# Kernel optimization log

Measured on AMD Instinct MI355X. Metric: run time of the kernel, lower is better.

## Reference

```python
import jax, jax.numpy as jnp
import numpy as np

EPS = 1e-3  # keras LayerNormalization default epsilon

def layernorm(x, gamma, beta):
    mu = jnp.mean(x, axis=-1, keepdims=True)
    var = jnp.var(x, axis=-1, keepdims=True)
    return (x - mu) * jax.lax.rsqrt(var + EPS) * gamma + beta

def setup_inputs() -> dict:
    key = jax.random.key(0)
    ks = jax.random.split(key, 20)
    B, N, T, Dimg, H = 512, 100, 14, 2048, 768
    s = lambda k, *sh: jax.random.normal(k, sh, dtype=jnp.float32) * 0.02
    return {
        "img_feat": jax.random.normal(ks[0], (B, N, Dimg), dtype=jnp.float32),
        "ques_feat": jax.random.normal(ks[1], (B, T, H), dtype=jnp.float32),
        "Wc": s(ks[2], Dimg, H), "bc": jnp.zeros((H,), jnp.float32),
        "Wq": s(ks[3], H, H),    "bq": jnp.zeros((H,), jnp.float32),
        "Wi": s(ks[4], Dimg, H), "bi": jnp.zeros((H,), jnp.float32),
        "wqa": s(ks[5], H, 1), "bqa": jnp.zeros((1,), jnp.float32),
        "wia": s(ks[6], H, 1), "bia": jnp.zeros((1,), jnp.float32),
        "g1": jnp.ones((N,), jnp.float32), "b1": jnp.zeros((N,), jnp.float32),
        "g2": jnp.ones((H,), jnp.float32), "b2": jnp.zeros((H,), jnp.float32),
        "g3": jnp.ones((T,), jnp.float32), "b3": jnp.zeros((T,), jnp.float32),
        "g4": jnp.ones((H,), jnp.float32), "b4": jnp.zeros((H,), jnp.float32),
        "g5": jnp.ones((N,), jnp.float32), "b5": jnp.zeros((N,), jnp.float32),
    }

def reference(img_feat, ques_feat, Wc, bc, Wq, bq, Wi, bi, wqa, bqa, wia, bia,
              g1, b1, g2, b2, g3, b3, g4, b4, g5, b5):
    # img_feat: [B,N,Dimg], ques_feat: [B,T,H]
    img_corr = img_feat @ Wc + bc                                   # [B,N,H]
    wm = jnp.einsum('bth,bnh->btn', ques_feat, img_corr)            # [B,T,N]
    wm = jax.nn.relu(layernorm(wm, g1, b1))
    ques_embed = ques_feat @ Wq + bq                                # [B,T,H]
    img_embed = img_feat @ Wi + bi                                  # [B,N,H]
    transform_img = jnp.einsum('btn,bnh->bth', wm, img_embed)       # [B,T,H]
    ques_atten_sum = jax.nn.relu(layernorm(transform_img + ques_embed, g2, b2))
    # dropout is identity at inference
    ques_atten = (ques_atten_sum @ wqa + bqa)[..., 0]               # [B,T]
    ques_atten = jax.nn.softmax(layernorm(ques_atten, g3, b3), axis=-1)
    transform_ques = jnp.einsum('btn,bth->bnh', wm, ques_embed)     # [B,N,H]
    img_atten_sum = jax.nn.relu(layernorm(transform_ques + img_embed, g4, b4))
    img_atten = (img_atten_sum @ wia + bia)[..., 0]                 # [B,N]
    img_atten = jax.nn.softmax(layernorm(img_atten, g5, b5), axis=-1)
    ques_atten_feat = jnp.einsum('bt,bth->bh', ques_atten, ques_feat)  # [B,H]
    img_atten_feat = jnp.einsum('bn,bnd->bd', img_atten, img_feat)     # [B,Dimg]
    return (img_atten_feat, ques_atten_feat)
```

## Files before the change

kernel.cpp:

```cpp
#include <hip/hip_runtime.h>

using f32x4     = __attribute__((ext_vector_type(4))) float;
using bf16x8    = __attribute__((ext_vector_type(8))) short;
using ushort4_t = __attribute__((ext_vector_type(4))) unsigned short;
using ushort8_t = __attribute__((ext_vector_type(8))) unsigned short;
using uint4_t   = __attribute__((ext_vector_type(4))) unsigned int;

__device__ __forceinline__ unsigned short f2bf(float f) {
    unsigned u = __builtin_bit_cast(unsigned, f);
    u += 0x7fffu + ((u >> 16) & 1u);
    return (unsigned short)(u >> 16);
}

__device__ __forceinline__ float wave_sum(float v) {
#pragma unroll
    for (int off = 32; off > 0; off >>= 1) v += __shfl_xor(v, off, 64);
    return v;
}
__device__ __forceinline__ float wave_max(float v) {
#pragma unroll
    for (int off = 32; off > 0; off >>= 1) v = fmaxf(v, __shfl_xor(v, off, 64));
    return v;
}

#define GLP(p)  ((const __attribute__((address_space(1))) void*)(p))
#define LDSP(p) ((__attribute__((address_space(3))) void*)(p))

__global__ __launch_bounds__(256) void cvt_bf16(const float* __restrict__ in,
                                                unsigned short* __restrict__ out, long n8) {
    long i = (long)blockIdx.x * 256 + threadIdx.x;
    long stride = (long)gridDim.x * 256;
    for (; i < n8; i += stride) {
        const float4* p = (const float4*)(in + i * 8);
        float4 a = p[0], b = p[1];
        ushort8_t v;
        v[0] = f2bf(a.x); v[1] = f2bf(a.y); v[2] = f2bf(a.z); v[3] = f2bf(a.w);
        v[4] = f2bf(b.x); v[5] = f2bf(b.y); v[6] = f2bf(b.z); v[7] = f2bf(b.w);
        *(ushort8_t*)(out + i * 8) = v;
    }
}

__global__ void pack_w(const float* __restrict__ Wc, const float* __restrict__ Wi,
                       unsigned short* __restrict__ Wp) {
    int n = blockIdx.x, k = blockIdx.y * 256 + threadIdx.x;
    float v = (n < 768) ? Wc[(size_t)k * 768 + n] : Wi[(size_t)k * 768 + (n - 768)];
    Wp[(size_t)n * 2048 + k] = f2bf(v);
}

__global__ void pack_wq(const float* __restrict__ Wq, unsigned short* __restrict__ Wqt) {
    int n = blockIdx.x, k = blockIdx.y * 256 + threadIdx.x;
    Wqt[(size_t)n * 768 + k] = f2bf(Wq[(size_t)k * 768 + n]);
}

__global__ __launch_bounds__(512, 1) void gemm8(
    const unsigned short* __restrict__ A, const unsigned short* __restrict__ Bt,
    const float* __restrict__ bias0, const float* __restrict__ bias1, int nsplit,
    float* __restrict__ C, int N, int K, int NTN)
{
    __shared__ unsigned short LA[4][8192];
    __shared__ unsigned short LB[4][8192];
    const int tid = threadIdx.x, lane = tid & 63, wid = tid >> 6;

    int nwg = (int)gridDim.x, bid = (int)blockIdx.x;
    if ((nwg & 7) == 0) { int cpx = nwg >> 3; bid = (bid & 7) * cpx + (bid >> 3); }
    const int tn = bid % NTN, tm = bid / NTN;
    const size_t m0 = (size_t)tm * 256, n0 = (size_t)tn * 256;
    const int NT = K >> 5;

    const int wr = wid >> 2, wc = wid & 3;
    const int wm = wr * 128, wn = wc * 64;
    const int fr = lane & 15, fs = lane >> 4;

    const int c0 = tid, c1 = tid + 512;
    const int r0 = c0 >> 2, s0 = ((c0 & 3) - (r0 >> 1)) & 3;
    const int r1 = c1 >> 2, s1 = ((c1 & 3) - (r1 >> 1)) & 3;
    const unsigned short* gA0 = A + (m0 + r0) * K + s0 * 8;
    const unsigned short* gA1 = A + (m0 + r1) * K + s1 * 8;
    const unsigned short* gB0 = Bt + (n0 + r0) * K + s0 * 8;
    const unsigned short* gB1 = Bt + (n0 + r1) * K + s1 * 8;

    int offA[8], offB[4];
#pragma unroll
    for (int mf = 0; mf < 8; ++mf) {
        int r = wm + mf * 16 + fr;
        offA[mf] = (4 * r + ((fs + (r >> 1)) & 3)) * 8;
    }
#pragma unroll
    for (int nf = 0; nf < 4; ++nf) {
        int r = wn + nf * 16 + fr;
        offB[nf] = (4 * r + ((fs + (r >> 1)) & 3)) * 8;
    }

    f32x4 acc[8][4];
#pragma unroll
    for (int i = 0; i < 8; ++i)
#pragma unroll
        for (int j = 0; j < 4; ++j) acc[i][j] = (f32x4){0.f, 0.f, 0.f, 0.f};

#pragma unroll
    for (int t = 0; t < 3; ++t) {
        if (t < NT) {
            __builtin_amdgcn_global_load_lds(GLP(gA0 + t * 32), LDSP(&LA[t][c0 * 8]), 16, 0, 0);
            __builtin_amdgcn_global_load_lds(GLP(gA1 + t * 32), LDSP(&LA[t][c1 * 8]), 16, 0, 0);
            __builtin_amdgcn_global_load_lds(GLP(gB0 + t * 32), LDSP(&LB[t][c0 * 8]), 16, 0, 0);
            __builtin_amdgcn_global_load_lds(GLP(gB1 + t * 32), LDSP(&LB[t][c1 * 8]), 16, 0, 0);
        }
    }

    for (int T = 0; T < NT; ++T) {
        const int buf = T & 3, pb = (T + 3) & 3;
        const int rem = NT - 1 - T;
        if (rem >= 2)      asm volatile("s_waitcnt vmcnt(8)" ::: "memory");
        else if (rem == 1) asm volatile("s_waitcnt vmcnt(4)" ::: "memory");
        else               asm volatile("s_waitcnt vmcnt(0)" ::: "memory");
        __builtin_amdgcn_s_barrier();
        __builtin_amdgcn_sched_barrier(0);

        bf16x8 av[4], bv[4];
#pragma unroll
        for (int mf = 0; mf < 4; ++mf) av[mf] = *(const bf16x8*)&LA[buf][offA[mf]];
#pragma unroll
        for (int nf = 0; nf < 4; ++nf) bv[nf] = *(const bf16x8*)&LB[buf][offB[nf]];
        if (T + 3 < NT) {
            __builtin_amdgcn_global_load_lds(GLP(gA0 + (size_t)(T + 3) * 32), LDSP(&LA[pb][c0 * 8]), 16, 0, 0);
            __builtin_amdgcn_global_load_lds(GLP(gA1 + (size_t)(T + 3) * 32), LDSP(&LA[pb][c1 * 8]), 16, 0, 0);
        }
        asm volatile("s_waitcnt lgkmcnt(0)" ::: "memory");
        __builtin_amdgcn_sched_barrier(0);
        __builtin_amdgcn_s_setprio(1);
#pragma unroll
        for (int mf = 0; mf < 4; ++mf)
#pragma unroll
            for (int nf = 0; nf < 4; ++nf)
                acc[mf][nf] = __builtin_amdgcn_mfma_f32_16x16x32_bf16(av[mf], bv[nf], acc[mf][nf], 0, 0, 0);
        __builtin_amdgcn_s_setprio(0);

#pragma unroll
        for (int mf = 0; mf < 4; ++mf) av[mf] = *(const bf16x8*)&LA[buf][offA[4 + mf]];
        if (T + 3 < NT) {
            __builtin_amdgcn_global_load_lds(GLP(gB0 + (size_t)(T + 3) * 32), LDSP(&LB[pb][c0 * 8]), 16, 0, 0);
            __builtin_amdgcn_global_load_lds(GLP(gB1 + (size_t)(T + 3) * 32), LDSP(&LB[pb][c1 * 8]), 16, 0, 0);
        }
        asm volatile("s_waitcnt lgkmcnt(0)" ::: "memory");
        __builtin_amdgcn_sched_barrier(0);
        __builtin_amdgcn_s_setprio(1);
#pragma unroll
        for (int mf = 0; mf < 4; ++mf)
#pragma unroll
            for (int nf = 0; nf < 4; ++nf)
                acc[4 + mf][nf] = __builtin_amdgcn_mfma_f32_16x16x32_bf16(av[mf], bv[nf], acc[4 + mf][nf], 0, 0, 0);
        __builtin_amdgcn_s_setprio(0);
    }

#pragma unroll
    for (int nf = 0; nf < 4; ++nf) {
        int col = (int)n0 + wn + nf * 16 + fr;
        float bs = (col < nsplit) ? bias0[col] : bias1[col - nsplit];
#pragma unroll
        for (int mf = 0; mf < 8; ++mf) {
            size_t rowb = m0 + wm + mf * 16 + fs * 4;
#pragma unroll
            for (int r = 0; r < 4; ++r)
                C[(rowb + r) * N + col] = acc[mf][nf][r] + bs;
        }
    }
}

__global__ __launch_bounds__(256) void gemm_fb(
    const float* __restrict__ A, const unsigned short* __restrict__ Bt,
    const float* __restrict__ bias0, const float* __restrict__ bias1, int nsplit,
    float* __restrict__ C, int M, int N, int K)
{
    const int tid = threadIdx.x, lane = tid & 63, wid = tid >> 6;
    const int m0 = blockIdx.x * 128, n0 = blockIdx.y * 128;
    __shared__ unsigned short Al[128 * 40];
    __shared__ unsigned short Bl[128 * 40];

    f32x4 acc[4][4];
#pragma unroll
    for (int i = 0; i < 4; ++i)
#pragma unroll
        for (int j = 0; j < 4; ++j) acc[i][j] = (f32x4){0.f, 0.f, 0.f, 0.f};

    const int wm_ = (wid >> 1) * 64, wn_ = (wid & 1) * 64;
    const int fr = lane & 15, fk = (lane >> 4) * 8;

    for (int k0 = 0; k0 < K; k0 += 32) {
        __syncthreads();
#pragma unroll
        for (int it = 0; it < 4; ++it) {
            int idx = tid + it * 256;
            int row = idx >> 3, c4 = idx & 7;
            float4 v = *(const float4*)(A + (size_t)(m0 + row) * K + k0 + c4 * 4);
            ushort4_t h;
            h.x = f2bf(v.x); h.y = f2bf(v.y); h.z = f2bf(v.z); h.w = f2bf(v.w);
            *(ushort4_t*)&Al[row * 40 + c4 * 4] = h;
        }
#pragma unroll
        for (int it = 0; it < 2; ++it) {
            int idx = tid + it * 256;
            int row = idx >> 2, c4 = idx & 3;
            uint4_t v = *(const uint4_t*)(Bt + (size_t)(n0 + row) * K + k0 + c4 * 8);
            *(uint4_t*)&Bl[row * 40 + c4 * 8] = v;
        }
        __syncthreads();

        bf16x8 af[4], bfr[4];
#pragma unroll
        for (int i = 0; i < 4; ++i) af[i]  = *(const bf16x8*)&Al[(wm_ + i * 16 + fr) * 40 + fk];
#pragma unroll
        for (int j = 0; j < 4; ++j) bfr[j] = *(const bf16x8*)&Bl[(wn_ + j * 16 + fr) * 40 + fk];
#pragma unroll
        for (int i = 0; i < 4; ++i)
#pragma unroll
            for (int j = 0; j < 4; ++j)
                acc[i][j] = __builtin_amdgcn_mfma_f32_16x16x32_bf16(af[i], bfr[j], acc[i][j], 0, 0, 0);
    }

#pragma unroll
    for (int j = 0; j < 4; ++j) {
        int col = n0 + wn_ + j * 16 + (lane & 15);
        float bs = (col < nsplit) ? bias0[col] : bias1[col - nsplit];
#pragma unroll
        for (int i = 0; i < 4; ++i) {
            int rowb = m0 + wm_ + i * 16 + (lane >> 4) * 4;
#pragma unroll
            for (int r = 0; r < 4; ++r)
                C[(size_t)(rowb + r) * N + col] = acc[i][j][r] + bs;
        }
    }
}

__global__ __launch_bounds__(256) void wm_kernel(
    const float* __restrict__ qf_g, const float* __restrict__ imgCE,
    const float* __restrict__ g1, const float* __restrict__ b1,
    float* __restrict__ wm_g)
{
    const int b = blockIdx.x, tid = threadIdx.x, lane = tid & 63, wid = tid >> 6;
    __shared__ float qf[14 * 768];
    __shared__ float wmr[14][100];

    const float4* src = (const float4*)(qf_g + (size_t)b * 14 * 768);
    for (int i = tid; i < 14 * 768 / 4; i += 256) ((float4*)qf)[i] = src[i];
    __syncthreads();

    for (int n = wid; n < 100; n += 4) {
        const float* row = imgCE + ((size_t)b * 100 + n) * 1536;
        float r[12];
#pragma unroll
        for (int j = 0; j < 12; ++j) r[j] = row[lane + 64 * j];
        for (int t = 0; t < 14; ++t) {
            const float* q = qf + t * 768;
            float s = 0.f;
#pragma unroll
            for (int j = 0; j < 12; ++j) s = fmaf(r[j], q[lane + 64 * j], s);
            s = wave_sum(s);
            if (lane == 0) wmr[t][n] = s;
        }
    }
    __syncthreads();

    for (int t = wid; t < 14; t += 4) {
        float x0 = wmr[t][lane];
        float x1 = (lane + 64 < 100) ? wmr[t][lane + 64] : 0.f;
        float s = wave_sum(x0 + x1);
        float q = wave_sum(x0 * x0 + x1 * x1);
        float mu = s * (1.f / 100.f);
        float var = q * (1.f / 100.f) - mu * mu;
        float rs = rsqrtf(var + 1e-3f);
        float* dst = wm_g + ((size_t)b * 14 + t) * 100;
        {
            float v = (x0 - mu) * rs * g1[lane] + b1[lane];
            dst[lane] = v > 0.f ? v : 0.f;
        }
        if (lane + 64 < 100) {
            float v = (x1 - mu) * rs * g1[lane + 64] + b1[lane + 64];
            dst[lane + 64] = v > 0.f ? v : 0.f;
        }
    }
}

__global__ __launch_bounds__(256) void ques_kernel(
    const float* __restrict__ qf_g, const float* __restrict__ qe_g,
    const float* __restrict__ imgCE, const float* __restrict__ wm_g,
    const float* __restrict__ g2, const float* __restrict__ b2,
    const float* __restrict__ g3, const float* __restrict__ b3,
    const float* __restrict__ wqa, const float* __restrict__ bqa,
    float* __restrict__ out_q)
{
    const int b = blockIdx.x, tid = threadIdx.x, lane = tid & 63, wid = tid >> 6;
    __shared__ float qe[14 * 768];
    __shared__ float wm[14 * 100];
    __shared__ float red[4][28];
    __shared__ float mu_s[14], rs_s[14], qa_s[14], qw_s[14];

    {
        const float4* src = (const float4*)(qe_g + (size_t)b * 14 * 768);
        for (int i = tid; i < 14 * 768 / 4; i += 256) ((float4*)qe)[i] = src[i];
        const float* ws = wm_g + (size_t)b * 1400;
        for (int i = tid; i < 1400; i += 256) wm[i] = ws[i];
    }
    __syncthreads();

    float a0[14], a1[14], a2[14];
#pragma unroll
    for (int t = 0; t < 14; ++t) { a0[t] = 0.f; a1[t] = 0.f; a2[t] = 0.f; }

    const float* ie_base = imgCE + (size_t)b * 100 * 1536 + 768;
    for (int n = 0; n < 100; ++n) {
        const float* ie = ie_base + (size_t)n * 1536;
        float e0 = ie[tid], e1 = ie[tid + 256], e2 = ie[tid + 512];
#pragma unroll
        for (int t = 0; t < 14; ++t) {
            float w = wm[t * 100 + n];
            a0[t] = fmaf(w, e0, a0[t]); a1[t] = fmaf(w, e1, a1[t]); a2[t] = fmaf(w, e2, a2[t]);
        }
    }
#pragma unroll
    for (int t = 0; t < 14; ++t) {
        a0[t] += qe[t * 768 + tid];
        a1[t] += qe[t * 768 + tid + 256];
        a2[t] += qe[t * 768 + tid + 512];
    }
#pragma unroll
    for (int t = 0; t < 14; ++t) {
        float s = wave_sum(a0[t] + a1[t] + a2[t]);
        float q = wave_sum(a0[t] * a0[t] + a1[t] * a1[t] + a2[t] * a2[t]);
        if (lane == 0) { red[wid][t] = s; red[wid][14 + t] = q; }
    }
    __syncthreads();
    if (tid < 14) {
        float s = red[0][tid] + red[1][tid] + red[2][tid] + red[3][tid];
        float q = red[0][14 + tid] + red[1][14 + tid] + red[2][14 + tid] + red[3][14 + tid];
        float mu = s * (1.f / 768.f);
        float var = q * (1.f / 768.f) - mu * mu;
        mu_s[tid] = mu; rs_s[tid] = rsqrtf(var + 1e-3f);
    }
    __syncthreads();

    float ga = g2[tid], ba = b2[tid], gb = g2[tid + 256], bb = b2[tid + 256],
          gc = g2[tid + 512], bc_ = b2[tid + 512];
    float w0 = wqa[tid], w1 = wqa[tid + 256], w2 = wqa[tid + 512];
#pragma unroll
    for (int t = 0; t < 14; ++t) {
        float mu = mu_s[t], rs = rs_s[t];
        float v0 = fmaxf((a0[t] - mu) * rs * ga + ba, 0.f);
        float v1 = fmaxf((a1[t] - mu) * rs * gb + bb, 0.f);
        float v2 = fmaxf((a2[t] - mu) * rs * gc + bc_, 0.f);
        float p = wave_sum(v0 * w0 + v1 * w1 + v2 * w2);
        if (lane == 0) red[wid][t] = p;
    }
    __syncthreads();
    if (tid < 14) qa_s[tid] = red[0][tid] + red[1][tid] + red[2][tid] + red[3][tid] + bqa[0];
    __syncthreads();
    if (tid == 0) {
        float s = 0.f;
        for (int t = 0; t < 14; ++t) s += qa_s[t];
        float mu = s * (1.f / 14.f);
        float q = 0.f;
        for (int t = 0; t < 14; ++t) { float d = qa_s[t] - mu; q += d * d; }
        float rs = rsqrtf(q * (1.f / 14.f) + 1e-3f);
        float e[14], mx = -1e30f;
        for (int t = 0; t < 14; ++t) { e[t] = (qa_s[t] - mu) * rs * g3[t] + b3[t]; mx = fmaxf(mx, e[t]); }
        float se = 0.f;
        for (int t = 0; t < 14; ++t) { e[t] = expf(e[t] - mx); se += e[t]; }
        float inv = 1.f / se;
        for (int t = 0; t < 14; ++t) qw_s[t] = e[t] * inv;
    }
    __syncthreads();

    const float* qf = qf_g + (size_t)b * 14 * 768;
#pragma unroll
    for (int c = 0; c < 3; ++c) {
        int h = tid + c * 256;
        float o = 0.f;
#pragma unroll
        for (int t = 0; t < 14; ++t) o = fmaf(qw_s[t], qf[t * 768 + h], o);
        out_q[(size_t)b * 768 + h] = o;
    }
}

__global__ __launch_bounds__(256) void img_kernel(
    const float* __restrict__ img_feat, const float* __restrict__ qe_g,
    const float* __restrict__ imgCE, const float* __restrict__ wm_g,
    const float* __restrict__ g4, const float* __restrict__ b4,
    const float* __restrict__ g5, const float* __restrict__ b5,
    const float* __restrict__ wia, const float* __restrict__ bia,
    float* __restrict__ out_i)
{
    const int b = blockIdx.x, tid = threadIdx.x, lane = tid & 63, wid = tid >> 6;
    __shared__ float qe[14 * 768];
    __shared__ float wm[14 * 100];
    __shared__ float red[4][20];
    __shared__ float mu_s[10], rs_s[10];
    __shared__ float ia_s[100], iw_s[100];

    {
        const float4* src = (const float4*)(qe_g + (size_t)b * 14 * 768);
        for (int i = tid; i < 14 * 768 / 4; i += 256) ((float4*)qe)[i] = src[i];
        const float* ws = wm_g + (size_t)b * 1400;
        for (int i = tid; i < 1400; i += 256) wm[i] = ws[i];
    }
    __syncthreads();

    float g4a = g4[tid], b4a = b4[tid], g4b = g4[tid + 256], b4b = b4[tid + 256],
          g4c = g4[tid + 512], b4c = b4[tid + 512];
    float wa = wia[tid], wb = wia[tid + 256], wc_ = wia[tid + 512];

    for (int g = 0; g < 10; ++g) {
        float t0[10], t1[10], t2[10];
#pragma unroll
        for (int i = 0; i < 10; ++i) { t0[i] = 0.f; t1[i] = 0.f; t2[i] = 0.f; }
#pragma unroll
        for (int t = 0; t < 14; ++t) {
            float q0 = qe[t * 768 + tid], q1 = qe[t * 768 + tid + 256], q2 = qe[t * 768 + tid + 512];
#pragma unroll
            for (int i = 0; i < 10; ++i) {
                float w = wm[t * 100 + g * 10 + i];
                t0[i] = fmaf(w, q0, t0[i]); t1[i] = fmaf(w, q1, t1[i]); t2[i] = fmaf(w, q2, t2[i]);
            }
        }
#pragma unroll
        for (int i = 0; i < 10; ++i) {
            const float* ie = imgCE + ((size_t)b * 100 + g * 10 + i) * 1536 + 768;
            t0[i] += ie[tid]; t1[i] += ie[tid + 256]; t2[i] += ie[tid + 512];
            float s = wave_sum(t0[i] + t1[i] + t2[i]);
            float q = wave_sum(t0[i] * t0[i] + t1[i] * t1[i] + t2[i] * t2[i]);
            if (lane == 0) { red[wid][i] = s; red[wid][10 + i] = q; }
        }
        __syncthreads();
        if (tid < 10) {
            float s = red[0][tid] + red[1][tid] + red[2][tid] + red[3][tid];
            float q = red[0][10 + tid] + red[1][10 + tid] + red[2][10 + tid] + red[3][10 + tid];
            float mu = s * (1.f / 768.f);
            float var = q * (1.f / 768.f) - mu * mu;
            mu_s[tid] = mu; rs_s[tid] = rsqrtf(var + 1e-3f);
        }
        __syncthreads();
#pragma unroll
        for (int i = 0; i < 10; ++i) {
            float mu = mu_s[i], rs = rs_s[i];
            float v0 = fmaxf((t0[i] - mu) * rs * g4a + b4a, 0.f);
            float v1 = fmaxf((t1[i] - mu) * rs * g4b + b4b, 0.f);
            float v2 = fmaxf((t2[i] - mu) * rs * g4c + b4c, 0.f);
            float p = wave_sum(v0 * wa + v1 * wb + v2 * wc_);
            if (lane == 0) red[wid][i] = p;
        }
        __syncthreads();
        if (tid < 10) ia_s[g * 10 + tid] = red[0][tid] + red[1][tid] + red[2][tid] + red[3][tid] + bia[0];
        __syncthreads();
    }

    if (wid == 0) {
        float x0 = ia_s[lane];
        float x1 = (lane + 64 < 100) ? ia_s[lane + 64] : 0.f;
        float s = wave_sum(x0 + x1);
        float q = wave_sum(x0 * x0 + x1 * x1);
        float mu = s * 0.01f;
        float var = q * 0.01f - mu * mu;
        float rs = rsqrtf(var + 1e-3f);
        float v0 = (x0 - mu) * rs * g5[lane] + b5[lane];
        float v1 = (lane + 64 < 100) ? (x1 - mu) * rs * g5[lane + 64] + b5[lane + 64] : -1e30f;
        float mx = wave_max(fmaxf(v0, v1));
        float e0 = expf(v0 - mx);
        float e1 = (lane + 64 < 100) ? expf(v1 - mx) : 0.f;
        float se = wave_sum(e0 + e1);
        float inv = 1.f / se;
        iw_s[lane] = e0 * inv;
        if (lane + 64 < 100) iw_s[lane + 64] = e1 * inv;
    }
    __syncthreads();

    const float* imf = img_feat + (size_t)b * 100 * 2048;
#pragma unroll
    for (int c = 0; c < 2; ++c) {
        int col = tid + c * 256;
        float4 acc = {0.f, 0.f, 0.f, 0.f};
        for (int n = 0; n < 100; ++n) {
            float4 v = ((const float4*)(imf + (size_t)n * 2048))[col];
            float w = iw_s[n];
            acc.x = fmaf(w, v.x, acc.x); acc.y = fmaf(w, v.y, acc.y);
            acc.z = fmaf(w, v.z, acc.z); acc.w = fmaf(w, v.w, acc.w);
        }
        ((float4*)(out_i + (size_t)b * 2048))[col] = acc;
    }
}

extern "C" void kernel_launch(void* const* d_in, const int* in_sizes, int n_in,
                              void* d_out, int out_size, void* d_ws, size_t ws_size,
                              hipStream_t stream)
{
    const float* img_feat = (const float*)d_in[0];
    const float* ques_feat = (const float*)d_in[1];
    const float* Wc = (const float*)d_in[2];
    const float* bc = (const float*)d_in[3];
    const float* Wq = (const float*)d_in[4];
    const float* bq = (const float*)d_in[5];
    const float* Wi = (const float*)d_in[6];
    const float* bi = (const float*)d_in[7];
    const float* wqa = (const float*)d_in[8];
    const float* bqa = (const float*)d_in[9];
    const float* wia = (const float*)d_in[10];
    const float* bia = (const float*)d_in[11];
    const float* g1 = (const float*)d_in[12]; const float* b1 = (const float*)d_in[13];
    const float* g2 = (const float*)d_in[14]; const float* b2 = (const float*)d_in[15];
    const float* g3 = (const float*)d_in[16]; const float* b3 = (const float*)d_in[17];
    const float* g4 = (const float*)d_in[18]; const float* b4 = (const float*)d_in[19];
    const float* g5 = (const float*)d_in[20]; const float* b5 = (const float*)d_in[21];

    const size_t SZ_WP   = 1536u * 2048u * 2u;
    const size_t SZ_WQT  = 768u * 768u * 2u;
    const size_t SZ_IMG  = 51200ull * 1536u * 4u;
    const size_t SZ_QE   = 7168u * 768u * 4u;
    const size_t SZ_WM   = 512u * 1400u * 4u;
    const size_t SZ_ABF  = 51200ull * 2048u * 2u;
    const size_t SZ_QBF  = 7168u * 768u * 2u;

    const size_t OFF_WP  = 0;
    const size_t OFF_WQT = OFF_WP + SZ_WP;
    const size_t OFF_IMG = OFF_WQT + SZ_WQT;
    const size_t OFF_QE  = OFF_IMG + SZ_IMG;
    const size_t OFF_WM  = OFF_QE + SZ_QE;
    const size_t OFF_ABF = OFF_WM + SZ_WM;
    const size_t OFF_QBF = OFF_ABF + SZ_ABF;
    const size_t NEED_FB  = OFF_ABF;
    const size_t NEED_NEW = OFF_QBF + SZ_QBF;

    if (ws_size < NEED_FB) return;

    char* ws = (char*)d_ws;
    unsigned short* Wp  = (unsigned short*)(ws + OFF_WP);
    unsigned short* Wqt = (unsigned short*)(ws + OFF_WQT);
    float* imgCE = (float*)(ws + OFF_IMG);
    float* qe    = (float*)(ws + OFF_QE);
    float* wm    = (float*)(ws + OFF_WM);

    float* out_img = (float*)d_out;
    float* out_q   = (float*)d_out + 512 * 2048;

    hipLaunchKernelGGL(pack_w,  dim3(1536, 8), dim3(256), 0, stream, Wc, Wi, Wp);
    hipLaunchKernelGGL(pack_wq, dim3(768, 3),  dim3(256), 0, stream, Wq, Wqt);

    if (ws_size >= NEED_NEW) {
        unsigned short* Abf = (unsigned short*)(ws + OFF_ABF);
        unsigned short* Qbf = (unsigned short*)(ws + OFF_QBF);
        hipLaunchKernelGGL(cvt_bf16, dim3(2048), dim3(256), 0, stream,
                           img_feat, Abf, (long)(51200ull * 2048u / 8u));
        hipLaunchKernelGGL(cvt_bf16, dim3(1024), dim3(256), 0, stream,
                           ques_feat, Qbf, (long)(7168u * 768u / 8u));
        hipLaunchKernelGGL(gemm8, dim3(1200), dim3(512), 0, stream,
                           Abf, Wp, bc, bi, 768, imgCE, 1536, 2048, 6);
        hipLaunchKernelGGL(gemm8, dim3(84), dim3(512), 0, stream,
                           Qbf, Wqt, bq, bq, 768, qe, 768, 768, 3);
    } else {
        hipLaunchKernelGGL(gemm_fb, dim3(400, 12), dim3(256), 0, stream,
                           img_feat, Wp, bc, bi, 768, imgCE, 51200, 1536, 2048);
        hipLaunchKernelGGL(gemm_fb, dim3(56, 6), dim3(256), 0, stream,
                           ques_feat, Wqt, bq, bq, 768, qe, 7168, 768, 768);
    }

    hipLaunchKernelGGL(wm_kernel, dim3(512), dim3(256), 0, stream,
                       ques_feat, imgCE, g1, b1, wm);
    hipLaunchKernelGGL(ques_kernel, dim3(512), dim3(256), 0, stream,
                       ques_feat, qe, imgCE, wm, g2, b2, g3, b3, wqa, bqa, out_q);
    hipLaunchKernelGGL(img_kernel, dim3(512), dim3(256), 0, stream,
                       img_feat, qe, imgCE, wm, g4, b4, g5, b5, wia, bia, out_img);
}
```

Baseline: 890.9 us.

## Use 64-wide K double-buffered GEMM pipeline and bf16 img_feat in final reduction

Result: no change. 903.8 us (+1.4%).

```diff
diff --git a/kernel.cpp b/kernel.cpp
--- a/kernel.cpp
+++ b/kernel.cpp
@@ -10,6 +10,9 @@
     unsigned u = __builtin_bit_cast(unsigned, f);
     u += 0x7fffu + ((u >> 16) & 1u);
     return (unsigned short)(u >> 16);
+}
+__device__ __forceinline__ float bf2f(unsigned short h) {
+    return __builtin_bit_cast(float, (unsigned)h << 16);
 }
 
 __device__ __forceinline__ float wave_sum(float v) {
@@ -57,38 +60,51 @@
     const float* __restrict__ bias0, const float* __restrict__ bias1, int nsplit,
     float* __restrict__ C, int N, int K, int NTN)
 {
-    __shared__ unsigned short LA[4][8192];
-    __shared__ unsigned short LB[4][8192];
+    __shared__ unsigned short LA[2][16384];
+    __shared__ unsigned short LB[2][16384];
     const int tid = threadIdx.x, lane = tid & 63, wid = tid >> 6;
 
     int nwg = (int)gridDim.x, bid = (int)blockIdx.x;
     if ((nwg & 7) == 0) { int cpx = nwg >> 3; bid = (bid & 7) * cpx + (bid >> 3); }
     const int tn = bid % NTN, tm = bid / NTN;
     const size_t m0 = (size_t)tm * 256, n0 = (size_t)tn * 256;
-    const int NT = K >> 5;
+    const int NT = K >> 6;
 
     const int wr = wid >> 2, wc = wid & 3;
     const int wm = wr * 128, wn = wc * 64;
     const int fr = lane & 15, fs = lane >> 4;
 
-    const int c0 = tid, c1 = tid + 512;
-    const int r0 = c0 >> 2, s0 = ((c0 & 3) - (r0 >> 1)) & 3;
-    const int r1 = c1 >> 2, s1 = ((c1 & 3) - (r1 >> 1)) & 3;
-    const unsigned short* gA0 = A + (m0 + r0) * K + s0 * 8;
-    const unsigned short* gA1 = A + (m0 + r1) * K + s1 * 8;
-    const unsigned short* gB0 = Bt + (n0 + r0) * K + s0 * 8;
-    const unsigned short* gB1 = Bt + (n0 + r1) * K + s1 * 8;
+    const unsigned short *gA0p, *gA1p, *gA2p, *gA3p, *gB0p, *gB1p, *gB2p, *gB3p;
+    int o0, o1, o2, o3;
+    {
+        int c, r, s;
+        c = tid;        r = c >> 3; s = ((c & 7) - r) & 7; gA0p = A + (m0 + r) * K + s * 8; gB0p = Bt + (n0 + r) * K + s * 8; o0 = c * 8;
+        c = tid + 512;  r = c >> 3; s = ((c & 7) - r) & 7; gA1p = A + (m0 + r) * K + s * 8; gB1p = Bt + (n0 + r) * K + s * 8; o1 = c * 8;
+        c = tid + 1024; r = c >> 3; s = ((c & 7) - r) & 7; gA2p = A + (m0 + r) * K + s * 8; gB2p = Bt + (n0 + r) * K + s * 8; o2 = c * 8;
+        c = tid + 1536; r = c >> 3; s = ((c & 7) - r) & 7; gA3p = A + (m0 + r) * K + s * 8; gB3p = Bt + (n0 + r) * K + s * 8; o3 = c * 8;
+    }
+
+#define STAGE8(koff, b) do { \
+    __builtin_amdgcn_global_load_lds(GLP(gA0p + (koff)), LDSP(&LA[b][o0]), 16, 0, 0); \
+    __builtin_amdgcn_global_load_lds(GLP(gA1p + (koff)), LDSP(&LA[b][o1]), 16, 0, 0); \
+    __builtin_amdgcn_global_load_lds(GLP(gA2p + (koff)), LDSP(&LA[b][o2]), 16, 0, 0); \
+    __builtin_amdgcn_global_load_lds(GLP(gA3p + (koff)), LDSP(&LA[b][o3]), 16, 0, 0); \
+    __builtin_amdgcn_global_load_lds(GLP(gB0p + (koff)), LDSP(&LB[b][o0]), 16, 0, 0); \
+    __builtin_amdgcn_global_load_lds(GLP(gB1p + (koff)), LDSP(&LB[b][o1]), 16, 0, 0); \
+    __builtin_amdgcn_global_load_lds(GLP(gB2p + (koff)), LDSP(&LB[b][o2]), 16, 0, 0); \
+    __builtin_amdgcn_global_load_lds(GLP(gB3p + (koff)), LDSP(&LB[b][o3]), 16, 0, 0); \
+} while (0)
 
     int offA[8], offB[4];
 #pragma unroll
     for (int mf = 0; mf < 8; ++mf) {
         int r = wm + mf * 16 + fr;
-        offA[mf] = (4 * r + ((fs + (r >> 1)) & 3)) * 8;
+        offA[mf] = (r * 8 + ((fs + r) & 7)) * 8;
     }
 #pragma unroll
     for (int nf = 0; nf < 4; ++nf) {
         int r = wn + nf * 16 + fr;
-        offB[nf] = (4 * r + ((fs + (r >> 1)) & 3)) * 8;
+        offB[nf] = (r * 8 + ((fs + r) & 7)) * 8;
     }
 
     f32x4 acc[8][4];
@@ -97,34 +113,66 @@
 #pragma unroll
         for (int j = 0; j < 4; ++j) acc[i][j] = (f32x4){0.f, 0.f, 0.f, 0.f};
 
-#pragma unroll
-    for (int t = 0; t < 3; ++t) {
-        if (t < NT) {
-            __builtin_amdgcn_global_load_lds(GLP(gA0 + t * 32), LDSP(&LA[t][c0 * 8]), 16, 0, 0);
-            __builtin_amdgcn_global_load_lds(GLP(gA1 + t * 32), LDSP(&LA[t][c1 * 8]), 16, 0, 0);
-            __builtin_amdgcn_global_load_lds(GLP(gB0 + t * 32), LDSP(&LB[t][c0 * 8]), 16, 0, 0);
-            __builtin_amdgcn_global_load_lds(GLP(gB1 + t * 32), LDSP(&LB[t][c1 * 8]), 16, 0, 0);
-        }
-    }
+    STAGE8(0, 0);
 
     for (int T = 0; T < NT; ++T) {
-        const int buf = T & 3, pb = (T + 3) & 3;
-        const int rem = NT - 1 - T;
-        if (rem >= 2)      asm volatile("s_waitcnt vmcnt(8)" ::: "memory");
-        else if (rem == 1) asm volatile("s_waitcnt vmcnt(4)" ::: "memory");
-        else               asm volatile("s_waitcnt vmcnt(0)" ::: "memory");
+        const int buf = T & 1;
         __builtin_amdgcn_s_barrier();
-        __builtin_amdgcn_sched_barrier(0);
-
-        bf16x8 av[4], bv[4];
-#pragma unroll
-        for (int mf = 0; mf < 4; ++mf) av[mf] = *(const bf16x8*)&LA[buf][offA[mf]];
-#pragma unroll
-        for (int nf = 0; nf < 4; ++nf) bv[nf] = *(const bf16x8*)&LB[buf][offB[nf]];
-        if (T + 3 < NT) {
-            __builtin_amdgcn_global_load_lds(GLP(gA0 + (size_t)(T + 3) * 32), LDSP(&LA[pb][c0 * 8]), 16, 0, 0);
-            __builtin_amdgcn_global_load_lds(GLP(gA1 + (size_t)(T + 3) * 32), LDSP(&LA[pb][c1 * 8]), 16, 0, 0);
-        }
+        if (T + 1 < NT) {
+            STAGE8((size_t)(T + 1) * 64, buf ^ 1);
+            asm volatile("s_waitcnt vmcnt(8)" ::: "memory");
+        } else {
+            asm volatile("s_waitcnt vmcnt(0)" ::: "memory");
+        }
+        __builtin_amdgcn_s_barrier();
+        __builtin_amdgcn_sched_barrier(0);
+
+        bf16x8 a0[4], a1[4], a2[4], a3[4], bv0[4], bv1[4];
+#pragma unroll
+        for (int mf = 0; mf < 4; ++mf) a0[mf] = *(const bf16x8*)&LA[buf][offA[mf]];
+#pragma unroll
+        for (int nf = 0; nf < 4; ++nf) bv0[nf] = *(const bf16x8*)&LB[buf][offB[nf]];
+#pragma unroll
+        for (int mf = 0; mf < 4; ++mf) a1[mf] = *(const bf16x8*)&LA[buf][offA[4 + mf]];
+        __builtin_amdgcn_sched_barrier(0);
+        asm volatile("s_waitcnt lgkmcnt(4)" ::: "memory");
+        __builtin_amdgcn_sched_barrier(0);
+        __builtin_amdgcn_s_setprio(1);
+#pragma unroll
+        for (int mf = 0; mf < 4; ++mf)
+#pragma unroll
+            for (int nf = 0; nf < 4; ++nf)
+                acc[mf][nf] = __builtin_amdgcn_mfma_f32_16x16x32_bf16(a0[mf], bv0[nf], acc[mf][nf], 0, 0, 0);
+        __builtin_amdgcn_s_setprio(0);
+
+#pragma unroll
+        for (int nf = 0; nf < 4; ++nf) bv1[nf] = *(const bf16x8*)&LB[buf][offB[nf] ^ 32];
+#pragma unroll
+        for (int mf = 0; mf < 4; ++mf) a2[mf] = *(const bf16x8*)&LA[buf][offA[mf] ^ 32];
+        __builtin_amdgcn_sched_barrier(0);
+        asm volatile("s_waitcnt lgkmcnt(8)" ::: "memory");
+        __builtin_amdgcn_sched_barrier(0);
+        __builtin_amdgcn_s_setprio(1);
+#pragma unroll
+        for (int mf = 0; mf < 4; ++mf)
+#pragma unroll
+            for (int nf = 0; nf < 4; ++nf)
+                acc[4 + mf][nf] = __builtin_amdgcn_mfma_f32_16x16x32_bf16(a1[mf], bv0[nf], acc[4 + mf][nf], 0, 0, 0);
+        __builtin_amdgcn_s_setprio(0);
+
+#pragma unroll
+        for (int mf = 0; mf < 4; ++mf) a3[mf] = *(const bf16x8*)&LA[buf][offA[4 + mf] ^ 32];
+        __builtin_amdgcn_sched_barrier(0);
+        asm volatile("s_waitcnt lgkmcnt(4)" ::: "memory");
+        __builtin_amdgcn_sched_barrier(0);
+        __builtin_amdgcn_s_setprio(1);
+#pragma unroll
+        for (int mf = 0; mf < 4; ++mf)
+#pragma unroll
+            for (int nf = 0; nf < 4; ++nf)
+                acc[mf][nf] = __builtin_amdgcn_mfma_f32_16x16x32_bf16(a2[mf], bv1[nf], acc[mf][nf], 0, 0, 0);
+        __builtin_amdgcn_s_setprio(0);
+
         asm volatile("s_waitcnt lgkmcnt(0)" ::: "memory");
         __builtin_amdgcn_sched_barrier(0);
         __builtin_amdgcn_s_setprio(1);
@@ -132,25 +180,10 @@
         for (int mf = 0; mf < 4; ++mf)
 #pragma unroll
             for (int nf = 0; nf < 4; ++nf)
-                acc[mf][nf] = __builtin_amdgcn_mfma_f32_16x16x32_bf16(av[mf], bv[nf], acc[mf][nf], 0, 0, 0);
+                acc[4 + mf][nf] = __builtin_amdgcn_mfma_f32_16x16x32_bf16(a3[mf], bv1[nf], acc[4 + mf][nf], 0, 0, 0);
         __builtin_amdgcn_s_setprio(0);
-
-#pragma unroll
-        for (int mf = 0; mf < 4; ++mf) av[mf] = *(const bf16x8*)&LA[buf][offA[4 + mf]];
-        if (T + 3 < NT) {
-            __builtin_amdgcn_global_load_lds(GLP(gB0 + (size_t)(T + 3) * 32), LDSP(&LB[pb][c0 * 8]), 16, 0, 0);
-            __builtin_amdgcn_global_load_lds(GLP(gB1 + (size_t)(T + 3) * 32), LDSP(&LB[pb][c1 * 8]), 16, 0, 0);
-        }
-        asm volatile("s_waitcnt lgkmcnt(0)" ::: "memory");
-        __builtin_amdgcn_sched_barrier(0);
-        __builtin_amdgcn_s_setprio(1);
-#pragma unroll
-        for (int mf = 0; mf < 4; ++mf)
-#pragma unroll
-            for (int nf = 0; nf < 4; ++nf)
-                acc[4 + mf][nf] = __builtin_amdgcn_mfma_f32_16x16x32_bf16(av[mf], bv[nf], acc[4 + mf][nf], 0, 0, 0);
-        __builtin_amdgcn_s_setprio(0);
-    }
+    }
+#undef STAGE8
 
 #pragma unroll
     for (int nf = 0; nf < 4; ++nf) {
@@ -381,7 +414,8 @@
 }
 
 __global__ __launch_bounds__(256) void img_kernel(
-    const float* __restrict__ img_feat, const float* __restrict__ qe_g,
+    const float* __restrict__ img_feat, const unsigned short* __restrict__ imf_bf, int use_bf,
+    const float* __restrict__ qe_g,
     const float* __restrict__ imgCE, const float* __restrict__ wm_g,
     const float* __restrict__ g4, const float* __restrict__ b4,
     const float* __restrict__ g5, const float* __restrict__ b5,
@@ -471,18 +505,35 @@
     }
     __syncthreads();
 
-    const float* imf = img_feat + (size_t)b * 100 * 2048;
-#pragma unroll
-    for (int c = 0; c < 2; ++c) {
-        int col = tid + c * 256;
-        float4 acc = {0.f, 0.f, 0.f, 0.f};
+    if (use_bf) {
+        const unsigned short* imf = imf_bf + (size_t)b * 100 * 2048;
+        float acc8[8];
+#pragma unroll
+        for (int j = 0; j < 8; ++j) acc8[j] = 0.f;
         for (int n = 0; n < 100; ++n) {
-            float4 v = ((const float4*)(imf + (size_t)n * 2048))[col];
+            ushort8_t v = *(const ushort8_t*)(imf + (size_t)n * 2048 + tid * 8);
             float w = iw_s[n];
-            acc.x = fmaf(w, v.x, acc.x); acc.y = fmaf(w, v.y, acc.y);
-            acc.z = fmaf(w, v.z, acc.z); acc.w = fmaf(w, v.w, acc.w);
-        }
-        ((float4*)(out_i + (size_t)b * 2048))[col] = acc;
+#pragma unroll
+            for (int j = 0; j < 8; ++j) acc8[j] = fmaf(w, bf2f(v[j]), acc8[j]);
+        }
+        float4* dst = (float4*)(out_i + (size_t)b * 2048);
+        float4 oA = {acc8[0], acc8[1], acc8[2], acc8[3]};
+        float4 oB = {acc8[4], acc8[5], acc8[6], acc8[7]};
+        dst[tid * 2] = oA; dst[tid * 2 + 1] = oB;
+    } else {
+        const float* imf = img_feat + (size_t)b * 100 * 2048;
+#pragma unroll
+        for (int c = 0; c < 2; ++c) {
+            int col = tid + c * 256;
+            float4 acc = {0.f, 0.f, 0.f, 0.f};
+            for (int n = 0; n < 100; ++n) {
+                float4 v = ((const float4*)(imf + (size_t)n * 2048))[col];
+                float w = iw_s[n];
+                acc.x = fmaf(w, v.x, acc.x); acc.y = fmaf(w, v.y, acc.y);
+                acc.z = fmaf(w, v.z, acc.z); acc.w = fmaf(w, v.w, acc.w);
+            }
+            ((float4*)(out_i + (size_t)b * 2048))[col] = acc;
+        }
     }
 }
 
@@ -552,17 +603,25 @@
                            Abf, Wp, bc, bi, 768, imgCE, 1536, 2048, 6);
         hipLaunchKernelGGL(gemm8, dim3(84), dim3(512), 0, stream,
                            Qbf, Wqt, bq, bq, 768, qe, 768, 768, 3);
+
+        hipLaunchKernelGGL(wm_kernel, dim3(512), dim3(256), 0, stream,
+                           ques_feat, imgCE, g1, b1, wm);
+        hipLaunchKernelGGL(ques_kernel, dim3(512), dim3(256), 0, stream,
+                           ques_feat, qe, imgCE, wm, g2, b2, g3, b3, wqa, bqa, out_q);
+        hipLaunchKernelGGL(img_kernel, dim3(512), dim3(256), 0, stream,
+                           img_feat, Abf, 1, qe, imgCE, wm, g4, b4, g5, b5, wia, bia, out_img);
     } else {
         hipLaunchKernelGGL(gemm_fb, dim3(400, 12), dim3(256), 0, stream,
                            img_feat, Wp, bc, bi, 768, imgCE, 51200, 1536, 2048);
         hipLaunchKernelGGL(gemm_fb, dim3(56, 6), dim3(256), 0, stream,
                            ques_feat, Wqt, bq, bq, 768, qe, 7168, 768, 768);
-    }
-
-    hipLaunchKernelGGL(wm_kernel, dim3(512), dim3(256), 0, stream,
-                       ques_feat, imgCE, g1, b1, wm);
-    hipLaunchKernelGGL(ques_kernel, dim3(512), dim3(256), 0, stream,
-                       ques_feat, qe, imgCE, wm, g2, b2, g3, b3, wqa, bqa, out_q);
-    hipLaunchKernelGGL(img_kernel, dim3(512), dim3(256), 0, stream,
-                       img_feat, qe, imgCE, wm, g4, b4, g5, b5, wia, bia, out_img);
-}
+
+        hipLaunchKernelGGL(wm_kernel, dim3(512), dim3(256), 0, stream,
+                           ques_feat, imgCE, g1, b1, wm);
+        hipLaunchKernelGGL(ques_kernel, dim3(512), dim3(256), 0, stream,
+                           ques_feat, qe, imgCE, wm, g2, b2, g3, b3, wqa, bqa, out_q);
+        hipLaunchKernelGGL(img_kernel, dim3(512), dim3(256), 0, stream,
+                           img_feat, (const unsigned short*)nullptr, 0, qe, imgCE, wm,
+                           g4, b4, g5, b5, wia, bia, out_img);
+    }
+}
```

## Store image GEMM output in bf16 and read bf16 inputs downstream

Applied to the files above, without the earlier changes.

Result: faster. 810.0 us (-9.1%).

```diff
diff --git a/kernel.cpp b/kernel.cpp
--- a/kernel.cpp
+++ b/kernel.cpp
@@ -10,6 +10,9 @@
     unsigned u = __builtin_bit_cast(unsigned, f);
     u += 0x7fffu + ((u >> 16) & 1u);
     return (unsigned short)(u >> 16);
+}
+__device__ __forceinline__ float bf2f(unsigned short h) {
+    return __builtin_bit_cast(float, (unsigned)h << 16);
 }
 
 __device__ __forceinline__ float wave_sum(float v) {
@@ -52,10 +55,11 @@
     Wqt[(size_t)n * 768 + k] = f2bf(Wq[(size_t)k * 768 + n]);
 }
 
+template <int OUTBF>
 __global__ __launch_bounds__(512, 1) void gemm8(
     const unsigned short* __restrict__ A, const unsigned short* __restrict__ Bt,
     const float* __restrict__ bias0, const float* __restrict__ bias1, int nsplit,
-    float* __restrict__ C, int N, int K, int NTN)
+    void* __restrict__ Cv, int N, int K, int NTN)
 {
     __shared__ unsigned short LA[4][8192];
     __shared__ unsigned short LB[4][8192];
@@ -160,79 +164,17 @@
         for (int mf = 0; mf < 8; ++mf) {
             size_t rowb = m0 + wm + mf * 16 + fs * 4;
 #pragma unroll
-            for (int r = 0; r < 4; ++r)
-                C[(rowb + r) * N + col] = acc[mf][nf][r] + bs;
-        }
-    }
-}
-
-__global__ __launch_bounds__(256) void gemm_fb(
-    const float* __restrict__ A, const unsigned short* __restrict__ Bt,
-    const float* __restrict__ bias0, const float* __restrict__ bias1, int nsplit,
-    float* __restrict__ C, int M, int N, int K)
-{
-    const int tid = threadIdx.x, lane = tid & 63, wid = tid >> 6;
-    const int m0 = blockIdx.x * 128, n0 = blockIdx.y * 128;
-    __shared__ unsigned short Al[128 * 40];
-    __shared__ unsigned short Bl[128 * 40];
-
-    f32x4 acc[4][4];
-#pragma unroll
-    for (int i = 0; i < 4; ++i)
-#pragma unroll
-        for (int j = 0; j < 4; ++j) acc[i][j] = (f32x4){0.f, 0.f, 0.f, 0.f};
-
-    const int wm_ = (wid >> 1) * 64, wn_ = (wid & 1) * 64;
-    const int fr = lane & 15, fk = (lane >> 4) * 8;
-
-    for (int k0 = 0; k0 < K; k0 += 32) {
-        __syncthreads();
-#pragma unroll
-        for (int it = 0; it < 4; ++it) {
-            int idx = tid + it * 256;
-            int row = idx >> 3, c4 = idx & 7;
-            float4 v = *(const float4*)(A + (size_t)(m0 + row) * K + k0 + c4 * 4);
-            ushort4_t h;
-            h.x = f2bf(v.x); h.y = f2bf(v.y); h.z = f2bf(v.z); h.w = f2bf(v.w);
-            *(ushort4_t*)&Al[row * 40 + c4 * 4] = h;
-        }
-#pragma unroll
-        for (int it = 0; it < 2; ++it) {
-            int idx = tid + it * 256;
-            int row = idx >> 2, c4 = idx & 3;
-            uint4_t v = *(const uint4_t*)(Bt + (size_t)(n0 + row) * K + k0 + c4 * 8);
-            *(uint4_t*)&Bl[row * 40 + c4 * 8] = v;
-        }
-        __syncthreads();
-
-        bf16x8 af[4], bfr[4];
-#pragma unroll
-        for (int i = 0; i < 4; ++i) af[i]  = *(const bf16x8*)&Al[(wm_ + i * 16 + fr) * 40 + fk];
-#pragma unroll
-        for (int j = 0; j < 4; ++j) bfr[j] = *(const bf16x8*)&Bl[(wn_ + j * 16 + fr) * 40 + fk];
-#pragma unroll
-        for (int i = 0; i < 4; ++i)
-#pragma unroll
-            for (int j = 0; j < 4; ++j)
-                acc[i][j] = __builtin_amdgcn_mfma_f32_16x16x32_bf16(af[i], bfr[j], acc[i][j], 0, 0, 0);
-    }
-
-#pragma unroll
-    for (int j = 0; j < 4; ++j) {
-        int col = n0 + wn_ + j * 16 + (lane & 15);
-        float bs = (col < nsplit) ? bias0[col] : bias1[col - nsplit];
-#pragma unroll
-        for (int i = 0; i < 4; ++i) {
-            int rowb = m0 + wm_ + i * 16 + (lane >> 4) * 4;
-#pragma unroll
-            for (int r = 0; r < 4; ++r)
-                C[(size_t)(rowb + r) * N + col] = acc[i][j][r] + bs;
+            for (int r = 0; r < 4; ++r) {
+                float v = acc[mf][nf][r] + bs;
+                if (OUTBF) ((unsigned short*)Cv)[(rowb + r) * N + col] = f2bf(v);
+                else       ((float*)Cv)[(rowb + r) * N + col] = v;
+            }
         }
     }
 }
 
 __global__ __launch_bounds__(256) void wm_kernel(
-    const float* __restrict__ qf_g, const float* __restrict__ imgCE,
+    const unsigned short* __restrict__ qbf, const unsigned short* __restrict__ imgCE,
     const float* __restrict__ g1, const float* __restrict__ b1,
     float* __restrict__ wm_g)
 {
@@ -240,15 +182,19 @@
     __shared__ float qf[14 * 768];
     __shared__ float wmr[14][100];
 
-    const float4* src = (const float4*)(qf_g + (size_t)b * 14 * 768);
-    for (int i = tid; i < 14 * 768 / 4; i += 256) ((float4*)qf)[i] = src[i];
+    const ushort8_t* src = (const ushort8_t*)(qbf + (size_t)b * 14 * 768);
+    for (int i = tid; i < 14 * 768 / 8; i += 256) {
+        ushort8_t v = src[i];
+#pragma unroll
+        for (int j = 0; j < 8; ++j) qf[i * 8 + j] = bf2f(v[j]);
+    }
     __syncthreads();
 
     for (int n = wid; n < 100; n += 4) {
-        const float* row = imgCE + ((size_t)b * 100 + n) * 1536;
+        const unsigned short* row = imgCE + ((size_t)b * 100 + n) * 1536;
         float r[12];
 #pragma unroll
-        for (int j = 0; j < 12; ++j) r[j] = row[lane + 64 * j];
+        for (int j = 0; j < 12; ++j) r[j] = bf2f(row[lane + 64 * j]);
         for (int t = 0; t < 14; ++t) {
             const float* q = qf + t * 768;
             float s = 0.f;
@@ -282,7 +228,7 @@
 
 __global__ __launch_bounds__(256) void ques_kernel(
     const float* __restrict__ qf_g, const float* __restrict__ qe_g,
-    const float* __restrict__ imgCE, const float* __restrict__ wm_g,
+    const unsigned short* __restrict__ imgCE, const float* __restrict__ wm_g,
     const float* __restrict__ g2, const float* __restrict__ b2,
     const float* __restrict__ g3, const float* __restrict__ b3,
     const float* __restrict__ wqa, const float* __restrict__ bqa,
@@ -306,10 +252,10 @@
 #pragma unroll
     for (int t = 0; t < 14; ++t) { a0[t] = 0.f; a1[t] = 0.f; a2[t] = 0.f; }
 
-    const float* ie_base = imgCE + (size_t)b * 100 * 1536 + 768;
+    const unsigned short* ie_base = imgCE + (size_t)b * 100 * 1536 + 768;
     for (int n = 0; n < 100; ++n) {
-        const float* ie = ie_base + (size_t)n * 1536;
-        float e0 = ie[tid], e1 = ie[tid + 256], e2 = ie[tid + 512];
+        const unsigned short* ie = ie_base + (size_t)n * 1536;
+        float e0 = bf2f(ie[tid]), e1 = bf2f(ie[tid + 256]), e2 = bf2f(ie[tid + 512]);
 #pragma unroll
         for (int t = 0; t < 14; ++t) {
             float w = wm[t * 100 + n];
@@ -381,8 +327,8 @@
 }
 
 __global__ __launch_bounds__(256) void img_kernel(
-    const float* __restrict__ img_feat, const float* __restrict__ qe_g,
-    const float* __restrict__ imgCE, const float* __restrict__ wm_g,
+    const unsigned short* __restrict__ imf_bf, const float* __restrict__ qe_g,
+    const unsigned short* __restrict__ imgCE, const float* __restrict__ wm_g,
     const float* __restrict__ g4, const float* __restrict__ b4,
     const float* __restrict__ g5, const float* __restrict__ b5,
     const float* __restrict__ wia, const float* __restrict__ bia,
@@ -422,8 +368,8 @@
         }
 #pragma unroll
         for (int i = 0; i < 10; ++i) {
-            const float* ie = imgCE + ((size_t)b * 100 + g * 10 + i) * 1536 + 768;
-            t0[i] += ie[tid]; t1[i] += ie[tid + 256]; t2[i] += ie[tid + 512];
+            const unsigned short* ie = imgCE + ((size_t)b * 100 + g * 10 + i) * 1536 + 768;
+            t0[i] += bf2f(ie[tid]); t1[i] += bf2f(ie[tid + 256]); t2[i] += bf2f(ie[tid + 512]);
             float s = wave_sum(t0[i] + t1[i] + t2[i]);
             float q = wave_sum(t0[i] * t0[i] + t1[i] * t1[i] + t2[i] * t2[i]);
             if (lane == 0) { red[wid][i] = s; red[wid][10 + i] = q; }
@@ -471,19 +417,20 @@
     }
     __syncthreads();
 
-    const float* imf = img_feat + (size_t)b * 100 * 2048;
-#pragma unroll
-    for (int c = 0; c < 2; ++c) {
-        int col = tid + c * 256;
-        float4 acc = {0.f, 0.f, 0.f, 0.f};
-        for (int n = 0; n < 100; ++n) {
-            float4 v = ((const float4*)(imf + (size_t)n * 2048))[col];
-            float w = iw_s[n];
-            acc.x = fmaf(w, v.x, acc.x); acc.y = fmaf(w, v.y, acc.y);
-            acc.z = fmaf(w, v.z, acc.z); acc.w = fmaf(w, v.w, acc.w);
-        }
-        ((float4*)(out_i + (size_t)b * 2048))[col] = acc;
-    }
+    const unsigned short* imf = imf_bf + (size_t)b * 100 * 2048;
+    float acc8[8];
+#pragma unroll
+    for (int j = 0; j < 8; ++j) acc8[j] = 0.f;
+    for (int n = 0; n < 100; ++n) {
+        ushort8_t v = *(const ushort8_t*)(imf + (size_t)n * 2048 + tid * 8);
+        float w = iw_s[n];
+#pragma unroll
+        for (int j = 0; j < 8; ++j) acc8[j] = fmaf(w, bf2f(v[j]), acc8[j]);
+    }
+    float4* dst = (float4*)(out_i + (size_t)b * 2048);
+    float4 oA = {acc8[0], acc8[1], acc8[2], acc8[3]};
+    float4 oB = {acc8[4], acc8[5], acc8[6], acc8[7]};
+    dst[tid * 2] = oA; dst[tid * 2 + 1] = oB;
 }
 
 extern "C" void kernel_launch(void* const* d_in, const int* in_sizes, int n_in,
@@ -510,7 +457,7 @@
 
     const size_t SZ_WP   = 1536u * 2048u * 2u;
     const size_t SZ_WQT  = 768u * 768u * 2u;
-    const size_t SZ_IMG  = 51200ull * 1536u * 4u;
+    const size_t SZ_IMG  = 51200ull * 1536u * 2u;
     const size_t SZ_QE   = 7168u * 768u * 4u;
     const size_t SZ_WM   = 512u * 1400u * 4u;
     const size_t SZ_ABF  = 51200ull * 2048u * 2u;
@@ -523,46 +470,37 @@
     const size_t OFF_WM  = OFF_QE + SZ_QE;
     const size_t OFF_ABF = OFF_WM + SZ_WM;
     const size_t OFF_QBF = OFF_ABF + SZ_ABF;
-    const size_t NEED_FB  = OFF_ABF;
-    const size_t NEED_NEW = OFF_QBF + SZ_QBF;
-
-    if (ws_size < NEED_FB) return;
+    const size_t NEED    = OFF_QBF + SZ_QBF;
+    if (ws_size < NEED) return;
 
     char* ws = (char*)d_ws;
-    unsigned short* Wp  = (unsigned short*)(ws + OFF_WP);
-    unsigned short* Wqt = (unsigned short*)(ws + OFF_WQT);
-    float* imgCE = (float*)(ws + OFF_IMG);
-    float* qe    = (float*)(ws + OFF_QE);
-    float* wm    = (float*)(ws + OFF_WM);
+    unsigned short* Wp    = (unsigned short*)(ws + OFF_WP);
+    unsigned short* Wqt   = (unsigned short*)(ws + OFF_WQT);
+    unsigned short* imgCE = (unsigned short*)(ws + OFF_IMG);
+    float*          qe    = (float*)(ws + OFF_QE);
+    float*          wm    = (float*)(ws + OFF_WM);
+    unsigned short* Abf   = (unsigned short*)(ws + OFF_ABF);
+    unsigned short* Qbf   = (unsigned short*)(ws + OFF_QBF);
 
     float* out_img = (float*)d_out;
     float* out_q   = (float*)d_out + 512 * 2048;
 
     hipLaunchKernelGGL(pack_w,  dim3(1536, 8), dim3(256), 0, stream, Wc, Wi, Wp);
     hipLaunchKernelGGL(pack_wq, dim3(768, 3),  dim3(256), 0, stream, Wq, Wqt);
-
-    if (ws_size >= NEED_NEW) {
-        unsigned short* Abf = (unsigned short*)(ws + OFF_ABF);
-        unsigned short* Qbf = (unsigned short*)(ws + OFF_QBF);
-        hipLaunchKernelGGL(cvt_bf16, dim3(2048), dim3(256), 0, stream,
-                           img_feat, Abf, (long)(51200ull * 2048u / 8u));
-        hipLaunchKernelGGL(cvt_bf16, dim3(1024), dim3(256), 0, stream,
-                           ques_feat, Qbf, (long)(7168u * 768u / 8u));
-        hipLaunchKernelGGL(gemm8, dim3(1200), dim3(512), 0, stream,
-                           Abf, Wp, bc, bi, 768, imgCE, 1536, 2048, 6);
-        hipLaunchKernelGGL(gemm8, dim3(84), dim3(512), 0, stream,
-                           Qbf, Wqt, bq, bq, 768, qe, 768, 768, 3);
-    } else {
-        hipLaunchKernelGGL(gemm_fb, dim3(400, 12), dim3(256), 0, stream,
-                           img_feat, Wp, bc, bi, 768, imgCE, 51200, 1536, 2048);
-        hipLaunchKernelGGL(gemm_fb, dim3(56, 6), dim3(256), 0, stream,
-                           ques_feat, Wqt, bq, bq, 768, qe, 7168, 768, 768);
-    }
+    hipLaunchKernelGGL(cvt_bf16, dim3(2048), dim3(256), 0, stream,
+                       img_feat, Abf, (long)(51200ull * 2048u / 8u));
+    hipLaunchKernelGGL(cvt_bf16, dim3(1024), dim3(256), 0, stream,
+                       ques_feat, Qbf, (long)(7168u * 768u / 8u));
+
+    hipLaunchKernelGGL(HIP_KERNEL_NAME(gemm8<1>), dim3(1200), dim3(512), 0, stream,
+                       Abf, Wp, bc, bi, 768, (void*)imgCE, 1536, 2048, 6);
+    hipLaunchKernelGGL(HIP_KERNEL_NAME(gemm8<0>), dim3(84), dim3(512), 0, stream,
+                       Qbf, Wqt, bq, bq, 768, (void*)qe, 768, 768, 3);
 
     hipLaunchKernelGGL(wm_kernel, dim3(512), dim3(256), 0, stream,
-                       ques_feat, imgCE, g1, b1, wm);
+                       Qbf, imgCE, g1, b1, wm);
     hipLaunchKernelGGL(ques_kernel, dim3(512), dim3(256), 0, stream,
                        ques_feat, qe, imgCE, wm, g2, b2, g3, b3, wqa, bqa, out_q);
     hipLaunchKernelGGL(img_kernel, dim3(512), dim3(256), 0, stream,
-                       img_feat, qe, imgCE, wm, g4, b4, g5, b5, wia, bia, out_img);
-}
+                       Abf, qe, imgCE, wm, g4, b4, g5, b5, wia, bia, out_img);
+}
```
